# Optimization experiments

Hardware: AMD Instinct MI355X
Metric: run time of the kernel (lower is better)

## Reference

```python
import jax, jax.numpy as jnp
import numpy as np

B, S, H = 2, 2048, 1024
NH, HD = 16, 64  # num heads, head dim


def setup_inputs() -> dict:
    key = jax.random.key(0)
    ks = jax.random.split(key, 8)
    scale = 0.02
    return {
        "hidden_states": jax.random.normal(ks[0], (B, S, H), dtype=jnp.float32),
        "attention_mask": jnp.zeros((B, 1, 1, S), dtype=jnp.float32),
        "Wq": jax.random.normal(ks[1], (H, H), dtype=jnp.float32) * scale,
        "bq": jnp.zeros((H,), dtype=jnp.float32),
        "Wk": jax.random.normal(ks[2], (H, H), dtype=jnp.float32) * scale,
        "bk": jnp.zeros((H,), dtype=jnp.float32),
        "Wv": jax.random.normal(ks[3], (H, H), dtype=jnp.float32) * scale,
        "bv": jnp.zeros((H,), dtype=jnp.float32),
    }


def _split_heads(x):
    # [B,S,H] -> [B,NH,S,HD]
    b, s, _ = x.shape
    return x.reshape(b, s, NH, HD).transpose(0, 2, 1, 3)


def reference(hidden_states, attention_mask, Wq, bq, Wk, bk, Wv, bv):
    q = _split_heads(hidden_states @ Wq.T + bq)
    k = _split_heads(hidden_states @ Wk.T + bk)
    v = _split_heads(hidden_states @ Wv.T + bv)
    # scores: [B,NH,S,S]
    scores = jnp.einsum("bhqd,bhkd->bhqk", q, k) / jnp.sqrt(jnp.float32(HD))
    scores = scores + attention_mask
    att = jax.nn.softmax(scores, axis=-1)  # dropout is identity in eval
    ctx = jnp.einsum("bhqk,bhkd->bhqd", att, v)
    # [B,NH,S,HD] -> [B,S,H]
    return ctx.transpose(0, 2, 1, 3).reshape(hidden_states.shape[0], hidden_states.shape[1], NH * HD)
```

## Files before the change

kernel.cpp:

```cpp
#include <hip/hip_runtime.h>
#include <stdint.h>

#define BB 2
#define SS 2048
#define HH 1024
#define NH 16
#define HD 64

#define LOG2E 1.4426950408889634f
#define QSCALE (0.125f * LOG2E)

typedef short bfrag  __attribute__((ext_vector_type(8)));
typedef short bfrag4 __attribute__((ext_vector_type(4)));
typedef float f32x4  __attribute__((ext_vector_type(4)));

__device__ __forceinline__ short f2bf(float f) {
    union { float f; uint32_t u; } v; v.f = f;
    uint32_t r = (v.u + 0x7fffu + ((v.u >> 16) & 1u)) >> 16;
    return (short)r;
}

__device__ __forceinline__ uint32_t pack_bf16(float a, float b) {
#if __has_builtin(__builtin_amdgcn_cvt_pk_bf16_f32)
    auto t = __builtin_amdgcn_cvt_pk_bf16_f32(a, b);
    uint32_t u; __builtin_memcpy(&u, &t, 4);
    return u;
#else
    uint32_t ua = __float_as_uint(a) + 0x8000u;
    uint32_t ub = __float_as_uint(b) + 0x8000u;
    return __builtin_amdgcn_perm(ub, ua, 0x07060302u);
#endif
}

__global__ __launch_bounds__(256) void cvt_all(
    const float* __restrict__ X,  const float* __restrict__ Wq,
    const float* __restrict__ Wk, const float* __restrict__ Wv,
    const float* __restrict__ mask,
    short* __restrict__ Xb, short* __restrict__ Wcat,
    float* __restrict__ maskl)
{
    int i = blockIdx.x * 256 + threadIdx.x;
    if (i >= 1835008) {
        int off = i - 1835008;
        float4 f = ((const float4*)mask)[off];
        f.x *= LOG2E; f.y *= LOG2E; f.z *= LOG2E; f.w *= LOG2E;
        ((float4*)maskl)[off] = f;
        return;
    }
    const float* src; short* dst; int off;
    if (i < 1048576)      { src = X;  dst = Xb;                 off = i; }
    else if (i < 1310720) { src = Wq; dst = Wcat;               off = i - 1048576; }
    else if (i < 1572864) { src = Wk; dst = Wcat + 1048576;     off = i - 1310720; }
    else                  { src = Wv; dst = Wcat + 2097152;     off = i - 1572864; }
    float4 f = ((const float4*)src)[off];
    short4 s;
    s.x = f2bf(f.x); s.y = f2bf(f.y); s.z = f2bf(f.z); s.w = f2bf(f.w);
    ((short4*)dst)[off] = s;
}

__device__ __forceinline__ void gload_lds16(const void* g, void* lds) {
    __builtin_amdgcn_global_load_lds(
        (__attribute__((address_space(1))) void*)(uintptr_t)g,
        (__attribute__((address_space(3))) void*)(uintptr_t)lds,
        16, 0, 0);
}

__global__ __launch_bounds__(256, 3) void qkv_gemm(
    const short* __restrict__ X, const short* __restrict__ Wcat,
    const float* __restrict__ bq, const float* __restrict__ bk, const float* __restrict__ bv,
    short* __restrict__ Qo, short* __restrict__ Ko, short* __restrict__ Vo)
{
    __shared__ __align__(16) short smem[17408];

    const int tid  = threadIdx.x;
    const int wave = tid >> 6, lane = tid & 63;
    const int quad = lane >> 4, l15 = lane & 15;
    const int mTile = blockIdx.y * 128;
    const int nTile = blockIdx.x * 128;
    const int z = nTile >> 10;
    const int nLocT = nTile & 1023;
    const float* bias = (z == 0) ? bq : (z == 1) ? bk : bv;

    f32x4 acc[4][4];
#pragma unroll
    for (int i = 0; i < 4; ++i)
#pragma unroll
        for (int j = 0; j < 4; ++j) acc[i][j] = (f32x4)0.0f;

    const int srow  = lane >> 3;
    const int c_lin = lane & 7;
    const int mBase = (wave >> 1) * 64;
    const int nBase = (wave & 1) * 64;

    for (int k0 = 0; k0 < 1024; k0 += 64) {
        __syncthreads();
#pragma unroll
        for (int i = 0; i < 4; ++i) {
            int row = i * 32 + wave * 8 + srow;
            int cg  = c_lin ^ (row & 7);
            gload_lds16(X + (size_t)(mTile + row) * 1024 + k0 + cg * 8,
                        (char*)smem + i * 4096 + wave * 1024);
            gload_lds16(Wcat + (size_t)(nTile + row) * 1024 + k0 + cg * 8,
                        (char*)smem + 16384 + i * 4096 + wave * 1024);
        }
        __syncthreads();

#pragma unroll
        for (int kt = 0; kt < 2; ++kt) {
            bfrag af[4], bf[4];
#pragma unroll
            for (int t = 0; t < 4; ++t) {
                int arow = mBase + t * 16 + l15;
                int aslot = (kt * 4 + quad) ^ (arow & 7);
                af[t] = *(const bfrag*)((const char*)smem + arow * 128 + aslot * 16);
                int brow = nBase + t * 16 + l15;
                int bslot = (kt * 4 + quad) ^ (brow & 7);
                bf[t] = *(const bfrag*)((const char*)smem + 16384 + brow * 128 + bslot * 16);
            }
#pragma unroll
            for (int mt = 0; mt < 4; ++mt)
#pragma unroll
                for (int ct = 0; ct < 4; ++ct)
                    acc[mt][ct] = __builtin_amdgcn_mfma_f32_16x16x32_bf16(
                        af[mt], bf[ct], acc[mt][ct], 0, 0, 0);
        }
    }

    __syncthreads();
    const int b = mTile >> 11, sBase = mTile & 2047;

    if (z == 2) {
#pragma unroll
        for (int mt = 0; mt < 4; ++mt)
#pragma unroll
            for (int ct = 0; ct < 4; ++ct)
#pragma unroll
                for (int r = 0; r < 4; ++r) {
                    int nl = nBase + ct * 16 + l15;
                    int sl = mBase + mt * 16 + quad * 4 + r;
                    smem[nl * 136 + sl] = f2bf(acc[mt][ct][r] + bias[nLocT + nl]);
                }
        __syncthreads();
#pragma unroll
        for (int p = 0; p < 8; ++p) {
            int nl = p * 16 + (tid >> 4);
            int cg = tid & 15;
            int blk = cg >> 3;
            int c2  = cg & 7;
            int base = blk * 64 + (c2 >> 2) * 32 + (c2 & 3) * 4;
            int2 lo = *(const int2*)(smem + nl * 136 + base);
            int2 hi = *(const int2*)(smem + nl * 136 + base + 16);
            int4 v; v.x = lo.x; v.y = lo.y; v.z = hi.x; v.w = hi.y;
            int ng = nLocT + nl, hh = ng >> 6, d = ng & 63;
            *(int4*)(Vo + ((size_t)(b * 16 + hh) * 64 + d) * 2048 + sBase + cg * 8) = v;
        }
    } else {
        short* Out = (z == 0) ? Qo : Ko;
        float scale = (z == 0) ? QSCALE : 1.0f;
#pragma unroll
        for (int mt = 0; mt < 4; ++mt)
#pragma unroll
            for (int ct = 0; ct < 4; ++ct)
#pragma unroll
                for (int r = 0; r < 4; ++r) {
                    int ml = mBase + mt * 16 + quad * 4 + r;
                    int nl = nBase + ct * 16 + l15;
                    smem[ml * 136 + nl] = f2bf((acc[mt][ct][r] + bias[nLocT + nl]) * scale);
                }
        __syncthreads();
#pragma unroll
        for (int p = 0; p < 8; ++p) {
            int ml = p * 16 + (tid >> 4);
            int c  = tid & 15;
            bfrag v8 = *(const bfrag*)(smem + ml * 136 + c * 8);
            int s  = sBase + ml;
            int nl = nLocT + c * 8, hh = nl >> 6, d = nl & 63;
            *(bfrag*)(Out + (((size_t)(b * 16 + hh) << 11) + s) * 64 + d) = v8;
        }
    }
}

__global__ __launch_bounds__(256, 2) void attn_kernel(
    const short* __restrict__ Qb, const short* __restrict__ Kb, const short* __restrict__ Vb,
    const float* __restrict__ maskl, float* __restrict__ out)
{
    __shared__ __align__(16) char smem[32768];

    const int tid  = threadIdx.x;
    const int wave = tid >> 6, lane = tid & 63;
    const int quad = lane >> 4, l15 = lane & 15;

    const int id = blockIdx.x;
    const int slot = id >> 3;
    const int bh = ((id & 7) << 2) | (slot & 3);
    const int qt = slot >> 2;
    const int b  = bh >> 4, h = bh & 15;
    const int qBase = qt * 128 + wave * 32;

    int ksrc[2], vsrc[2];
#pragma unroll
    for (int i = 0; i < 2; ++i) {
        int ci = wave * 128 + i * 64 + lane;
        int r = ci >> 3, c = ci & 7;
        int cs = (c ^ (r & 7)) * 16;
        ksrc[i] = r * 128  + cs;
        vsrc[i] = r * 4096 + cs;
    }
    const char* kBase = (const char*)(Kb + (size_t)bh * SS * HD);
    const char* vBase = (const char*)(Vb + (size_t)bh * HD * SS);
    const char* mSrc  = (const char*)(maskl + b * SS) + quad * 16;

    const short* Qp = Qb + ((size_t)bh * SS + qBase) * HD;
    bfrag qf[2][2];
#pragma unroll
    for (int hf = 0; hf < 2; ++hf)
#pragma unroll
        for (int kt = 0; kt < 2; ++kt)
            qf[hf][kt] = *(const bfrag*)(Qp + (size_t)(hf * 16 + l15) * HD + kt * 32 + quad * 8);

    int kAddr[2];
#pragma unroll
    for (int kt = 0; kt < 2; ++kt)
        kAddr[kt] = l15 * 128 + (((kt * 4 + quad) ^ (l15 & 7)) * 16);
    int vAddr[2];
#pragma unroll
    for (int g = 0; g < 2; ++g)
        vAddr[g] = 8192 + l15 * 128 + (((g * 4 + quad) ^ (l15 & 7)) * 16);

    const f32x4 z4 = (f32x4)0.0f;
    const bfrag ones8 = {0x3F80, 0x3F80, 0x3F80, 0x3F80,
                         0x3F80, 0x3F80, 0x3F80, 0x3F80};

    f32x4 oacc[2][4], ol[2];
#pragma unroll
    for (int hf = 0; hf < 2; ++hf) {
        ol[hf] = z4;
#pragma unroll
        for (int dt = 0; dt < 4; ++dt) oacc[hf][dt] = z4;
    }

#pragma unroll
    for (int i = 0; i < 2; ++i) {
        gload_lds16(kBase + ksrc[i], smem + wave * 2048 + i * 1024);
        gload_lds16(vBase + vsrc[i], smem + 8192 + wave * 2048 + i * 1024);
    }

    auto astep = [&](int CUR, int NXT, int jn, int pref) {
        __syncthreads();
        if (pref) {
#pragma unroll
            for (int i = 0; i < 2; ++i) {
                gload_lds16(kBase + jn * 8192 + ksrc[i], smem + NXT + wave * 2048 + i * 1024);
                gload_lds16(vBase + jn * 128  + vsrc[i], smem + NXT + 8192 + wave * 2048 + i * 1024);
            }
        }

        f32x4 mvl[4];
#pragma unroll
        for (int ct = 0; ct < 4; ++ct)
            mvl[ct] = *(const f32x4*)(mSrc + ct * 64);
        mSrc += 256;

        f32x4 s0[4], s1[4];
#pragma unroll
        for (int ct = 0; ct < 4; ++ct) {
            bfrag kf0 = *(const bfrag*)(smem + CUR + kAddr[0] + ct * 2048);
            bfrag kf1 = *(const bfrag*)(smem + CUR + kAddr[1] + ct * 2048);
            s0[ct] = __builtin_amdgcn_mfma_f32_16x16x32_bf16(kf0, qf[0][0], mvl[ct], 0, 0, 0);
            s0[ct] = __builtin_amdgcn_mfma_f32_16x16x32_bf16(kf1, qf[0][1], s0[ct],  0, 0, 0);
            s1[ct] = __builtin_amdgcn_mfma_f32_16x16x32_bf16(kf0, qf[1][0], mvl[ct], 0, 0, 0);
            s1[ct] = __builtin_amdgcn_mfma_f32_16x16x32_bf16(kf1, qf[1][1], s1[ct],  0, 0, 0);
        }

        bfrag p0[2], p1[2];
#pragma unroll
        for (int g = 0; g < 2; ++g) {
            union { uint32_t u[4]; bfrag v; } cvt;
            cvt.u[0] = pack_bf16(__builtin_amdgcn_exp2f(s0[2*g][0]),   __builtin_amdgcn_exp2f(s0[2*g][1]));
            cvt.u[1] = pack_bf16(__builtin_amdgcn_exp2f(s0[2*g][2]),   __builtin_amdgcn_exp2f(s0[2*g][3]));
            cvt.u[2] = pack_bf16(__builtin_amdgcn_exp2f(s0[2*g+1][0]), __builtin_amdgcn_exp2f(s0[2*g+1][1]));
            cvt.u[3] = pack_bf16(__builtin_amdgcn_exp2f(s0[2*g+1][2]), __builtin_amdgcn_exp2f(s0[2*g+1][3]));
            p0[g] = cvt.v;
            cvt.u[0] = pack_bf16(__builtin_amdgcn_exp2f(s1[2*g][0]),   __builtin_amdgcn_exp2f(s1[2*g][1]));
            cvt.u[1] = pack_bf16(__builtin_amdgcn_exp2f(s1[2*g][2]),   __builtin_amdgcn_exp2f(s1[2*g][3]));
            cvt.u[2] = pack_bf16(__builtin_amdgcn_exp2f(s1[2*g+1][0]), __builtin_amdgcn_exp2f(s1[2*g+1][1]));
            cvt.u[3] = pack_bf16(__builtin_amdgcn_exp2f(s1[2*g+1][2]), __builtin_amdgcn_exp2f(s1[2*g+1][3]));
            p1[g] = cvt.v;
        }

#pragma unroll
        for (int dt = 0; dt < 4; ++dt) {
#pragma unroll
            for (int g = 0; g < 2; ++g) {
                bfrag v = *(const bfrag*)(smem + CUR + vAddr[g] + dt * 2048);
                oacc[0][dt] = __builtin_amdgcn_mfma_f32_16x16x32_bf16(p0[g], v, oacc[0][dt], 0, 0, 0);
                oacc[1][dt] = __builtin_amdgcn_mfma_f32_16x16x32_bf16(p1[g], v, oacc[1][dt], 0, 0, 0);
            }
        }
#pragma unroll
        for (int g = 0; g < 2; ++g) {
            ol[0] = __builtin_amdgcn_mfma_f32_16x16x32_bf16(p0[g], ones8, ol[0], 0, 0, 0);
            ol[1] = __builtin_amdgcn_mfma_f32_16x16x32_bf16(p1[g], ones8, ol[1], 0, 0, 0);
        }
    };

    for (int jj = 0; jj < 16; ++jj) {
        astep(0,     16384, 2 * jj + 1, 1);
        astep(16384, 0,     2 * jj + 2, jj < 15);
    }

#pragma unroll
    for (int hf = 0; hf < 2; ++hf) {
#pragma unroll
        for (int r = 0; r < 4; ++r) {
            float linv = 1.0f / ol[hf][r];
            int qrow = qBase + hf * 16 + quad * 4 + r;
#pragma unroll
            for (int dt = 0; dt < 4; ++dt)
                out[((size_t)(b * SS + qrow)) * HH + h * 64 + dt * 16 + l15] =
                    oacc[hf][dt][r] * linv;
        }
    }
}

extern "C" void kernel_launch(void* const* d_in, const int* in_sizes, int n_in,
                              void* d_out, int out_size, void* d_ws, size_t ws_size,
                              hipStream_t stream) {
    const float* hs   = (const float*)d_in[0];
    const float* mask = (const float*)d_in[1];
    const float* Wq   = (const float*)d_in[2];
    const float* bq   = (const float*)d_in[3];
    const float* Wk   = (const float*)d_in[4];
    const float* bk   = (const float*)d_in[5];
    const float* Wv   = (const float*)d_in[6];
    const float* bv   = (const float*)d_in[7];
    float* out = (float*)d_out;

    char* ws = (char*)d_ws;
    short* Xb    = (short*)(ws);
    short* Wcat  = (short*)(ws + (8ull  << 20));
    short* Qb    = (short*)(ws + (14ull << 20));
    short* Kb    = (short*)(ws + (22ull << 20));
    short* Vb    = (short*)(ws + (30ull << 20));
    float* maskl = (float*)(ws + (38ull << 20));

    cvt_all<<<7172, 256, 0, stream>>>(hs, Wq, Wk, Wv, mask, Xb, Wcat, maskl);

    qkv_gemm<<<dim3(24, 32), 256, 0, stream>>>(Xb, Wcat, bq, bk, bv, Qb, Kb, Vb);

    attn_kernel<<<512, 256, 0, stream>>>(Qb, Kb, Vb, maskl, out);
}
```

Before: 157.9 us.

## Double KV tile to 128 keys per step and add MFMA priority hints

The attention kernel now processes 128 keys per pipeline step instead of 64. K/V shared tiles double to 64KB of LDS with a 16-way XOR swizzle for V, so half as many barriers and async prefetches are issued. It also wraps the MFMA phases in s_setprio to favour matrix issue, and batches V fragment loads ahead of their MFMAs. The larger LDS footprint (64KB per block) may limit the two-blocks-per-CU occupancy, and the extra live score registers raise register pressure.

```diff
diff --git a/kernel.cpp b/kernel.cpp
--- a/kernel.cpp
+++ b/kernel.cpp
@@ -184,7 +184,7 @@
     const short* __restrict__ Qb, const short* __restrict__ Kb, const short* __restrict__ Vb,
     const float* __restrict__ maskl, float* __restrict__ out)
 {
-    __shared__ __align__(16) char smem[32768];
+    __shared__ __align__(16) char smem[65536];
 
     const int tid  = threadIdx.x;
     const int wave = tid >> 6, lane = tid & 63;
@@ -197,14 +197,14 @@
     const int b  = bh >> 4, h = bh & 15;
     const int qBase = qt * 128 + wave * 32;
 
-    int ksrc[2], vsrc[2];
-#pragma unroll
-    for (int i = 0; i < 2; ++i) {
-        int ci = wave * 128 + i * 64 + lane;
-        int r = ci >> 3, c = ci & 7;
-        int cs = (c ^ (r & 7)) * 16;
-        ksrc[i] = r * 128  + cs;
-        vsrc[i] = r * 4096 + cs;
+    int ksrc[4], vsrc[4];
+#pragma unroll
+    for (int i = 0; i < 4; ++i) {
+        int ci = wave * 256 + i * 64 + lane;
+        int kr = ci >> 3, kc = ci & 7;
+        ksrc[i] = kr * 128 + ((kc ^ (kr & 7)) * 16);
+        int vr = ci >> 4, vc = ci & 15;
+        vsrc[i] = vr * 4096 + ((vc ^ (vr & 15)) * 16);
     }
     const char* kBase = (const char*)(Kb + (size_t)bh * SS * HD);
     const char* vBase = (const char*)(Vb + (size_t)bh * HD * SS);
@@ -222,10 +222,12 @@
 #pragma unroll
     for (int kt = 0; kt < 2; ++kt)
         kAddr[kt] = l15 * 128 + (((kt * 4 + quad) ^ (l15 & 7)) * 16);
-    int vAddr[2];
-#pragma unroll
-    for (int g = 0; g < 2; ++g)
-        vAddr[g] = 8192 + l15 * 128 + (((g * 4 + quad) ^ (l15 & 7)) * 16);
+    int vAddr[2][2];
+#pragma unroll
+    for (int a = 0; a < 2; ++a)
+#pragma unroll
+        for (int g = 0; g < 2; ++g)
+            vAddr[a][g] = 16384 + l15 * 256 + (((a * 8 + g * 4 + quad) ^ l15) * 16);
 
     const f32x4 z4 = (f32x4)0.0f;
     const bfrag ones8 = {0x3F80, 0x3F80, 0x3F80, 0x3F80,
@@ -240,73 +242,85 @@
     }
 
 #pragma unroll
-    for (int i = 0; i < 2; ++i) {
-        gload_lds16(kBase + ksrc[i], smem + wave * 2048 + i * 1024);
-        gload_lds16(vBase + vsrc[i], smem + 8192 + wave * 2048 + i * 1024);
+    for (int i = 0; i < 4; ++i) {
+        gload_lds16(kBase + ksrc[i], smem + wave * 4096 + i * 1024);
+        gload_lds16(vBase + vsrc[i], smem + 16384 + wave * 4096 + i * 1024);
     }
 
     auto astep = [&](int CUR, int NXT, int jn, int pref) {
         __syncthreads();
         if (pref) {
 #pragma unroll
-            for (int i = 0; i < 2; ++i) {
-                gload_lds16(kBase + jn * 8192 + ksrc[i], smem + NXT + wave * 2048 + i * 1024);
-                gload_lds16(vBase + jn * 128  + vsrc[i], smem + NXT + 8192 + wave * 2048 + i * 1024);
-            }
-        }
-
-        f32x4 mvl[4];
-#pragma unroll
-        for (int ct = 0; ct < 4; ++ct)
-            mvl[ct] = *(const f32x4*)(mSrc + ct * 64);
-        mSrc += 256;
-
-        f32x4 s0[4], s1[4];
-#pragma unroll
-        for (int ct = 0; ct < 4; ++ct) {
-            bfrag kf0 = *(const bfrag*)(smem + CUR + kAddr[0] + ct * 2048);
-            bfrag kf1 = *(const bfrag*)(smem + CUR + kAddr[1] + ct * 2048);
-            s0[ct] = __builtin_amdgcn_mfma_f32_16x16x32_bf16(kf0, qf[0][0], mvl[ct], 0, 0, 0);
-            s0[ct] = __builtin_amdgcn_mfma_f32_16x16x32_bf16(kf1, qf[0][1], s0[ct],  0, 0, 0);
-            s1[ct] = __builtin_amdgcn_mfma_f32_16x16x32_bf16(kf0, qf[1][0], mvl[ct], 0, 0, 0);
-            s1[ct] = __builtin_amdgcn_mfma_f32_16x16x32_bf16(kf1, qf[1][1], s1[ct],  0, 0, 0);
-        }
-
-        bfrag p0[2], p1[2];
-#pragma unroll
-        for (int g = 0; g < 2; ++g) {
-            union { uint32_t u[4]; bfrag v; } cvt;
-            cvt.u[0] = pack_bf16(__builtin_amdgcn_exp2f(s0[2*g][0]),   __builtin_amdgcn_exp2f(s0[2*g][1]));
-            cvt.u[1] = pack_bf16(__builtin_amdgcn_exp2f(s0[2*g][2]),   __builtin_amdgcn_exp2f(s0[2*g][3]));
-            cvt.u[2] = pack_bf16(__builtin_amdgcn_exp2f(s0[2*g+1][0]), __builtin_amdgcn_exp2f(s0[2*g+1][1]));
-            cvt.u[3] = pack_bf16(__builtin_amdgcn_exp2f(s0[2*g+1][2]), __builtin_amdgcn_exp2f(s0[2*g+1][3]));
-            p0[g] = cvt.v;
-            cvt.u[0] = pack_bf16(__builtin_amdgcn_exp2f(s1[2*g][0]),   __builtin_amdgcn_exp2f(s1[2*g][1]));
-            cvt.u[1] = pack_bf16(__builtin_amdgcn_exp2f(s1[2*g][2]),   __builtin_amdgcn_exp2f(s1[2*g][3]));
-            cvt.u[2] = pack_bf16(__builtin_amdgcn_exp2f(s1[2*g+1][0]), __builtin_amdgcn_exp2f(s1[2*g+1][1]));
-            cvt.u[3] = pack_bf16(__builtin_amdgcn_exp2f(s1[2*g+1][2]), __builtin_amdgcn_exp2f(s1[2*g+1][3]));
-            p1[g] = cvt.v;
-        }
-
-#pragma unroll
-        for (int dt = 0; dt < 4; ++dt) {
+            for (int i = 0; i < 4; ++i) {
+                gload_lds16(kBase + (size_t)jn * 16384 + ksrc[i],
+                            smem + NXT + wave * 4096 + i * 1024);
+                gload_lds16(vBase + (size_t)jn * 256 + vsrc[i],
+                            smem + NXT + 16384 + wave * 4096 + i * 1024);
+            }
+        }
+
+        f32x4 s0[2][4], s1[2][4];
+        __builtin_amdgcn_s_setprio(1);
+#pragma unroll
+        for (int a = 0; a < 2; ++a) {
+            f32x4 mvl[4];
+#pragma unroll
+            for (int ct = 0; ct < 4; ++ct)
+                mvl[ct] = *(const f32x4*)(mSrc + a * 256 + ct * 64);
+#pragma unroll
+            for (int ct = 0; ct < 4; ++ct) {
+                bfrag kf0 = *(const bfrag*)(smem + CUR + a * 8192 + kAddr[0] + ct * 2048);
+                bfrag kf1 = *(const bfrag*)(smem + CUR + a * 8192 + kAddr[1] + ct * 2048);
+                s0[a][ct] = __builtin_amdgcn_mfma_f32_16x16x32_bf16(kf0, qf[0][0], mvl[ct], 0, 0, 0);
+                s0[a][ct] = __builtin_amdgcn_mfma_f32_16x16x32_bf16(kf1, qf[0][1], s0[a][ct], 0, 0, 0);
+                s1[a][ct] = __builtin_amdgcn_mfma_f32_16x16x32_bf16(kf0, qf[1][0], mvl[ct], 0, 0, 0);
+                s1[a][ct] = __builtin_amdgcn_mfma_f32_16x16x32_bf16(kf1, qf[1][1], s1[a][ct], 0, 0, 0);
+            }
+        }
+        __builtin_amdgcn_s_setprio(0);
+        mSrc += 512;
+
+        bfrag p0[2][2], p1[2][2];
+#pragma unroll
+        for (int a = 0; a < 2; ++a)
 #pragma unroll
             for (int g = 0; g < 2; ++g) {
-                bfrag v = *(const bfrag*)(smem + CUR + vAddr[g] + dt * 2048);
-                oacc[0][dt] = __builtin_amdgcn_mfma_f32_16x16x32_bf16(p0[g], v, oacc[0][dt], 0, 0, 0);
-                oacc[1][dt] = __builtin_amdgcn_mfma_f32_16x16x32_bf16(p1[g], v, oacc[1][dt], 0, 0, 0);
-            }
-        }
-#pragma unroll
-        for (int g = 0; g < 2; ++g) {
-            ol[0] = __builtin_amdgcn_mfma_f32_16x16x32_bf16(p0[g], ones8, ol[0], 0, 0, 0);
-            ol[1] = __builtin_amdgcn_mfma_f32_16x16x32_bf16(p1[g], ones8, ol[1], 0, 0, 0);
-        }
+                union { uint32_t u[4]; bfrag v; } cvt;
+                cvt.u[0] = pack_bf16(__builtin_amdgcn_exp2f(s0[a][2*g][0]),   __builtin_amdgcn_exp2f(s0[a][2*g][1]));
+                cvt.u[1] = pack_bf16(__builtin_amdgcn_exp2f(s0[a][2*g][2]),   __builtin_amdgcn_exp2f(s0[a][2*g][3]));
+                cvt.u[2] = pack_bf16(__builtin_amdgcn_exp2f(s0[a][2*g+1][0]), __builtin_amdgcn_exp2f(s0[a][2*g+1][1]));
+                cvt.u[3] = pack_bf16(__builtin_amdgcn_exp2f(s0[a][2*g+1][2]), __builtin_amdgcn_exp2f(s0[a][2*g+1][3]));
+                p0[a][g] = cvt.v;
+                cvt.u[0] = pack_bf16(__builtin_amdgcn_exp2f(s1[a][2*g][0]),   __builtin_amdgcn_exp2f(s1[a][2*g][1]));
+                cvt.u[1] = pack_bf16(__builtin_amdgcn_exp2f(s1[a][2*g][2]),   __builtin_amdgcn_exp2f(s1[a][2*g][3]));
+                cvt.u[2] = pack_bf16(__builtin_amdgcn_exp2f(s1[a][2*g+1][0]), __builtin_amdgcn_exp2f(s1[a][2*g+1][1]));
+                cvt.u[3] = pack_bf16(__builtin_amdgcn_exp2f(s1[a][2*g+1][2]), __builtin_amdgcn_exp2f(s1[a][2*g+1][3]));
+                p1[a][g] = cvt.v;
+            }
+
+        __builtin_amdgcn_s_setprio(1);
+#pragma unroll
+        for (int a = 0; a < 2; ++a)
+#pragma unroll
+            for (int g = 0; g < 2; ++g) {
+                bfrag vv[4];
+#pragma unroll
+                for (int dt = 0; dt < 4; ++dt)
+                    vv[dt] = *(const bfrag*)(smem + CUR + vAddr[a][g] + dt * 4096);
+#pragma unroll
+                for (int dt = 0; dt < 4; ++dt) {
+                    oacc[0][dt] = __builtin_amdgcn_mfma_f32_16x16x32_bf16(p0[a][g], vv[dt], oacc[0][dt], 0, 0, 0);
+                    oacc[1][dt] = __builtin_amdgcn_mfma_f32_16x16x32_bf16(p1[a][g], vv[dt], oacc[1][dt], 0, 0, 0);
+                }
+                ol[0] = __builtin_amdgcn_mfma_f32_16x16x32_bf16(p0[a][g], ones8, ol[0], 0, 0, 0);
+                ol[1] = __builtin_amdgcn_mfma_f32_16x16x32_bf16(p1[a][g], ones8, ol[1], 0, 0, 0);
+            }
+        __builtin_amdgcn_s_setprio(0);
     };
 
-    for (int jj = 0; jj < 16; ++jj) {
-        astep(0,     16384, 2 * jj + 1, 1);
-        astep(16384, 0,     2 * jj + 2, jj < 15);
+    for (int jj = 0; jj < 8; ++jj) {
+        astep(0,     32768, 2 * jj + 1, 1);
+        astep(32768, 0,     2 * jj + 2, jj < 7);
     }
 
 #pragma unroll
```

Result: no change. 156.0 us (-1.2%).

## Halve attention query tile, double grid, stage mask in LDS, add setprio

Applied to the files above, without the earlier changes.

The attention kernel now handles 64 query rows per block (16 per wave) instead of 128, so the grid doubles to 1024 blocks and launch bounds allow 4 blocks per CU. The aim is more resident waves per CU to hide latency, and fewer registers per wave. The mask row is copied once into an extra 8 KB of LDS instead of being read from global memory every step. s_setprio is raised around the MFMA sections to favour matrix issue. In exchange, each K/V tile loaded into LDS serves half as many query rows, which doubles K/V global and LDS traffic per unit of work.

```diff
diff --git a/kernel.cpp b/kernel.cpp
--- a/kernel.cpp
+++ b/kernel.cpp
@@ -180,11 +180,11 @@
     }
 }
 
-__global__ __launch_bounds__(256, 2) void attn_kernel(
+__global__ __launch_bounds__(256, 4) void attn_kernel(
     const short* __restrict__ Qb, const short* __restrict__ Kb, const short* __restrict__ Vb,
     const float* __restrict__ maskl, float* __restrict__ out)
 {
-    __shared__ __align__(16) char smem[32768];
+    __shared__ __align__(16) char smem[40960];
 
     const int tid  = threadIdx.x;
     const int wave = tid >> 6, lane = tid & 63;
@@ -195,7 +195,7 @@
     const int bh = ((id & 7) << 2) | (slot & 3);
     const int qt = slot >> 2;
     const int b  = bh >> 4, h = bh & 15;
-    const int qBase = qt * 128 + wave * 32;
+    const int qBase = qt * 64 + wave * 16;
 
     int ksrc[2], vsrc[2];
 #pragma unroll
@@ -208,15 +208,12 @@
     }
     const char* kBase = (const char*)(Kb + (size_t)bh * SS * HD);
     const char* vBase = (const char*)(Vb + (size_t)bh * HD * SS);
-    const char* mSrc  = (const char*)(maskl + b * SS) + quad * 16;
 
     const short* Qp = Qb + ((size_t)bh * SS + qBase) * HD;
-    bfrag qf[2][2];
-#pragma unroll
-    for (int hf = 0; hf < 2; ++hf)
-#pragma unroll
-        for (int kt = 0; kt < 2; ++kt)
-            qf[hf][kt] = *(const bfrag*)(Qp + (size_t)(hf * 16 + l15) * HD + kt * 32 + quad * 8);
+    bfrag qf[2];
+#pragma unroll
+    for (int kt = 0; kt < 2; ++kt)
+        qf[kt] = *(const bfrag*)(Qp + (size_t)l15 * HD + kt * 32 + quad * 8);
 
     int kAddr[2];
 #pragma unroll
@@ -231,77 +228,77 @@
     const bfrag ones8 = {0x3F80, 0x3F80, 0x3F80, 0x3F80,
                          0x3F80, 0x3F80, 0x3F80, 0x3F80};
 
-    f32x4 oacc[2][4], ol[2];
-#pragma unroll
-    for (int hf = 0; hf < 2; ++hf) {
-        ol[hf] = z4;
-#pragma unroll
-        for (int dt = 0; dt < 4; ++dt) oacc[hf][dt] = z4;
-    }
+    f32x4 oacc[4], ol = z4;
+#pragma unroll
+    for (int dt = 0; dt < 4; ++dt) oacc[dt] = z4;
 
 #pragma unroll
     for (int i = 0; i < 2; ++i) {
         gload_lds16(kBase + ksrc[i], smem + wave * 2048 + i * 1024);
         gload_lds16(vBase + vsrc[i], smem + 8192 + wave * 2048 + i * 1024);
     }
+#pragma unroll
+    for (int i = 0; i < 2; ++i) {
+        int ci = wave * 128 + i * 64 + lane;
+        gload_lds16((const char*)(maskl + b * SS) + ci * 16,
+                    smem + 32768 + wave * 2048 + i * 1024);
+    }
+
+    int mOff = 32768 + quad * 16;
 
     auto astep = [&](int CUR, int NXT, int jn, int pref) {
         __syncthreads();
         if (pref) {
 #pragma unroll
             for (int i = 0; i < 2; ++i) {
-                gload_lds16(kBase + jn * 8192 + ksrc[i], smem + NXT + wave * 2048 + i * 1024);
-                gload_lds16(vBase + jn * 128  + vsrc[i], smem + NXT + 8192 + wave * 2048 + i * 1024);
+                gload_lds16(kBase + (size_t)jn * 8192 + ksrc[i],
+                            smem + NXT + wave * 2048 + i * 1024);
+                gload_lds16(vBase + (size_t)jn * 128 + vsrc[i],
+                            smem + NXT + 8192 + wave * 2048 + i * 1024);
             }
         }
 
         f32x4 mvl[4];
 #pragma unroll
         for (int ct = 0; ct < 4; ++ct)
-            mvl[ct] = *(const f32x4*)(mSrc + ct * 64);
-        mSrc += 256;
-
-        f32x4 s0[4], s1[4];
+            mvl[ct] = *(const f32x4*)(smem + mOff + ct * 64);
+        mOff += 256;
+
+        f32x4 s[4];
+        __builtin_amdgcn_s_setprio(1);
 #pragma unroll
         for (int ct = 0; ct < 4; ++ct) {
             bfrag kf0 = *(const bfrag*)(smem + CUR + kAddr[0] + ct * 2048);
             bfrag kf1 = *(const bfrag*)(smem + CUR + kAddr[1] + ct * 2048);
-            s0[ct] = __builtin_amdgcn_mfma_f32_16x16x32_bf16(kf0, qf[0][0], mvl[ct], 0, 0, 0);
-            s0[ct] = __builtin_amdgcn_mfma_f32_16x16x32_bf16(kf1, qf[0][1], s0[ct],  0, 0, 0);
-            s1[ct] = __builtin_amdgcn_mfma_f32_16x16x32_bf16(kf0, qf[1][0], mvl[ct], 0, 0, 0);
-            s1[ct] = __builtin_amdgcn_mfma_f32_16x16x32_bf16(kf1, qf[1][1], s1[ct],  0, 0, 0);
-        }
-
-        bfrag p0[2], p1[2];
+            s[ct] = __builtin_amdgcn_mfma_f32_16x16x32_bf16(kf0, qf[0], mvl[ct], 0, 0, 0);
+            s[ct] = __builtin_amdgcn_mfma_f32_16x16x32_bf16(kf1, qf[1], s[ct],  0, 0, 0);
+        }
+        __builtin_amdgcn_s_setprio(0);
+
+        bfrag p[2];
 #pragma unroll
         for (int g = 0; g < 2; ++g) {
             union { uint32_t u[4]; bfrag v; } cvt;
-            cvt.u[0] = pack_bf16(__builtin_amdgcn_exp2f(s0[2*g][0]),   __builtin_amdgcn_exp2f(s0[2*g][1]));
-            cvt.u[1] = pack_bf16(__builtin_amdgcn_exp2f(s0[2*g][2]),   __builtin_amdgcn_exp2f(s0[2*g][3]));
-            cvt.u[2] = pack_bf16(__builtin_amdgcn_exp2f(s0[2*g+1][0]), __builtin_amdgcn_exp2f(s0[2*g+1][1]));
-            cvt.u[3] = pack_bf16(__builtin_amdgcn_exp2f(s0[2*g+1][2]), __builtin_amdgcn_exp2f(s0[2*g+1][3]));
-            p0[g] = cvt.v;
-            cvt.u[0] = pack_bf16(__builtin_amdgcn_exp2f(s1[2*g][0]),   __builtin_amdgcn_exp2f(s1[2*g][1]));
-            cvt.u[1] = pack_bf16(__builtin_amdgcn_exp2f(s1[2*g][2]),   __builtin_amdgcn_exp2f(s1[2*g][3]));
-            cvt.u[2] = pack_bf16(__builtin_amdgcn_exp2f(s1[2*g+1][0]), __builtin_amdgcn_exp2f(s1[2*g+1][1]));
-            cvt.u[3] = pack_bf16(__builtin_amdgcn_exp2f(s1[2*g+1][2]), __builtin_amdgcn_exp2f(s1[2*g+1][3]));
-            p1[g] = cvt.v;
-        }
-
-#pragma unroll
-        for (int dt = 0; dt < 4; ++dt) {
-#pragma unroll
-            for (int g = 0; g < 2; ++g) {
-                bfrag v = *(const bfrag*)(smem + CUR + vAddr[g] + dt * 2048);
-                oacc[0][dt] = __builtin_amdgcn_mfma_f32_16x16x32_bf16(p0[g], v, oacc[0][dt], 0, 0, 0);
-                oacc[1][dt] = __builtin_amdgcn_mfma_f32_16x16x32_bf16(p1[g], v, oacc[1][dt], 0, 0, 0);
-            }
-        }
+            cvt.u[0] = pack_bf16(__builtin_amdgcn_exp2f(s[2*g][0]),   __builtin_amdgcn_exp2f(s[2*g][1]));
+            cvt.u[1] = pack_bf16(__builtin_amdgcn_exp2f(s[2*g][2]),   __builtin_amdgcn_exp2f(s[2*g][3]));
+            cvt.u[2] = pack_bf16(__builtin_amdgcn_exp2f(s[2*g+1][0]), __builtin_amdgcn_exp2f(s[2*g+1][1]));
+            cvt.u[3] = pack_bf16(__builtin_amdgcn_exp2f(s[2*g+1][2]), __builtin_amdgcn_exp2f(s[2*g+1][3]));
+            p[g] = cvt.v;
+        }
+
+        __builtin_amdgcn_s_setprio(1);
 #pragma unroll
         for (int g = 0; g < 2; ++g) {
-            ol[0] = __builtin_amdgcn_mfma_f32_16x16x32_bf16(p0[g], ones8, ol[0], 0, 0, 0);
-            ol[1] = __builtin_amdgcn_mfma_f32_16x16x32_bf16(p1[g], ones8, ol[1], 0, 0, 0);
-        }
+            bfrag vv[4];
+#pragma unroll
+            for (int dt = 0; dt < 4; ++dt)
+                vv[dt] = *(const bfrag*)(smem + CUR + vAddr[g] + dt * 2048);
+#pragma unroll
+            for (int dt = 0; dt < 4; ++dt)
+                oacc[dt] = __builtin_amdgcn_mfma_f32_16x16x32_bf16(p[g], vv[dt], oacc[dt], 0, 0, 0);
+            ol = __builtin_amdgcn_mfma_f32_16x16x32_bf16(p[g], ones8, ol, 0, 0, 0);
+        }
+        __builtin_amdgcn_s_setprio(0);
     };
 
     for (int jj = 0; jj < 16; ++jj) {
@@ -310,16 +307,13 @@
     }
 
 #pragma unroll
-    for (int hf = 0; hf < 2; ++hf) {
-#pragma unroll
-        for (int r = 0; r < 4; ++r) {
-            float linv = 1.0f / ol[hf][r];
-            int qrow = qBase + hf * 16 + quad * 4 + r;
-#pragma unroll
-            for (int dt = 0; dt < 4; ++dt)
-                out[((size_t)(b * SS + qrow)) * HH + h * 64 + dt * 16 + l15] =
-                    oacc[hf][dt][r] * linv;
-        }
+    for (int r = 0; r < 4; ++r) {
+        float linv = 1.0f / ol[r];
+        int qrow = qBase + quad * 4 + r;
+#pragma unroll
+        for (int dt = 0; dt < 4; ++dt)
+            out[((size_t)(b * SS + qrow)) * HH + h * 64 + dt * 16 + l15] =
+                oacc[dt][r] * linv;
     }
 }
 
@@ -348,5 +342,5 @@
 
     qkv_gemm<<<dim3(24, 32), 256, 0, stream>>>(Xb, Wcat, bq, bk, bv, Qb, Kb, Vb);
 
-    attn_kernel<<<512, 256, 0, stream>>>(Qb, Kb, Vb, maskl, out);
-}
+    attn_kernel<<<1024, 256, 0, stream>>>(Qb, Kb, Vb, maskl, out);
+}
```

Result: slower. 162.7 us (+3.1%).

## Split attention KV range across two wave groups per block with LDS reduction

Applied to the files above, without the earlier changes.

Doubles the attention block to 512 threads. The two 4-wave groups each process half of the key/value sequence for the same 128 query rows, using separate LDS double buffers, and their partial outputs and row sums are combined through LDS at the end. This doubles the number of waves available to hide latency without raising the grid size. It also raises wave priority around the MFMA sections. The cost is 64KB of LDS per block, an extra reduction pass, and possibly lower block occupancy per CU.

```diff
diff --git a/kernel.cpp b/kernel.cpp
--- a/kernel.cpp
+++ b/kernel.cpp
@@ -180,27 +180,32 @@
     }
 }
 
-__global__ __launch_bounds__(256, 2) void attn_kernel(
+__global__ __launch_bounds__(512, 4) void attn_kernel(
     const short* __restrict__ Qb, const short* __restrict__ Kb, const short* __restrict__ Vb,
     const float* __restrict__ maskl, float* __restrict__ out)
 {
-    __shared__ __align__(16) char smem[32768];
+    __shared__ __align__(16) char smem[65536];
 
     const int tid  = threadIdx.x;
     const int wave = tid >> 6, lane = tid & 63;
     const int quad = lane >> 4, l15 = lane & 15;
+    const int grp  = wave >> 2;
+    const int gw   = wave & 3;
 
     const int id = blockIdx.x;
     const int slot = id >> 3;
     const int bh = ((id & 7) << 2) | (slot & 3);
     const int qt = slot >> 2;
     const int b  = bh >> 4, h = bh & 15;
-    const int qBase = qt * 128 + wave * 32;
+    const int qBase = qt * 128 + gw * 32;
+
+    const int gBase = grp * 32768;
+    const int t0 = grp * 16;
 
     int ksrc[2], vsrc[2];
 #pragma unroll
     for (int i = 0; i < 2; ++i) {
-        int ci = wave * 128 + i * 64 + lane;
+        int ci = gw * 128 + i * 64 + lane;
         int r = ci >> 3, c = ci & 7;
         int cs = (c ^ (r & 7)) * 16;
         ksrc[i] = r * 128  + cs;
@@ -208,7 +213,7 @@
     }
     const char* kBase = (const char*)(Kb + (size_t)bh * SS * HD);
     const char* vBase = (const char*)(Vb + (size_t)bh * HD * SS);
-    const char* mSrc  = (const char*)(maskl + b * SS) + quad * 16;
+    const char* mSrc  = (const char*)(maskl + b * SS + grp * 1024) + quad * 16;
 
     const short* Qp = Qb + ((size_t)bh * SS + qBase) * HD;
     bfrag qf[2][2];
@@ -221,11 +226,11 @@
     int kAddr[2];
 #pragma unroll
     for (int kt = 0; kt < 2; ++kt)
-        kAddr[kt] = l15 * 128 + (((kt * 4 + quad) ^ (l15 & 7)) * 16);
+        kAddr[kt] = gBase + l15 * 128 + (((kt * 4 + quad) ^ (l15 & 7)) * 16);
     int vAddr[2];
 #pragma unroll
     for (int g = 0; g < 2; ++g)
-        vAddr[g] = 8192 + l15 * 128 + (((g * 4 + quad) ^ (l15 & 7)) * 16);
+        vAddr[g] = gBase + 8192 + l15 * 128 + (((g * 4 + quad) ^ (l15 & 7)) * 16);
 
     const f32x4 z4 = (f32x4)0.0f;
     const bfrag ones8 = {0x3F80, 0x3F80, 0x3F80, 0x3F80,
@@ -241,8 +246,8 @@
 
 #pragma unroll
     for (int i = 0; i < 2; ++i) {
-        gload_lds16(kBase + ksrc[i], smem + wave * 2048 + i * 1024);
-        gload_lds16(vBase + vsrc[i], smem + 8192 + wave * 2048 + i * 1024);
+        gload_lds16(kBase + (size_t)t0 * 8192 + ksrc[i], smem + gBase + gw * 2048 + i * 1024);
+        gload_lds16(vBase + (size_t)t0 * 128  + vsrc[i], smem + gBase + 8192 + gw * 2048 + i * 1024);
     }
 
     auto astep = [&](int CUR, int NXT, int jn, int pref) {
@@ -250,8 +255,10 @@
         if (pref) {
 #pragma unroll
             for (int i = 0; i < 2; ++i) {
-                gload_lds16(kBase + jn * 8192 + ksrc[i], smem + NXT + wave * 2048 + i * 1024);
-                gload_lds16(vBase + jn * 128  + vsrc[i], smem + NXT + 8192 + wave * 2048 + i * 1024);
+                gload_lds16(kBase + (size_t)jn * 8192 + ksrc[i],
+                            smem + gBase + NXT + gw * 2048 + i * 1024);
+                gload_lds16(vBase + (size_t)jn * 128  + vsrc[i],
+                            smem + gBase + NXT + 8192 + gw * 2048 + i * 1024);
             }
         }
 
@@ -262,6 +269,7 @@
         mSrc += 256;
 
         f32x4 s0[4], s1[4];
+        __builtin_amdgcn_s_setprio(1);
 #pragma unroll
         for (int ct = 0; ct < 4; ++ct) {
             bfrag kf0 = *(const bfrag*)(smem + CUR + kAddr[0] + ct * 2048);
@@ -271,6 +279,7 @@
             s1[ct] = __builtin_amdgcn_mfma_f32_16x16x32_bf16(kf0, qf[1][0], mvl[ct], 0, 0, 0);
             s1[ct] = __builtin_amdgcn_mfma_f32_16x16x32_bf16(kf1, qf[1][1], s1[ct],  0, 0, 0);
         }
+        __builtin_amdgcn_s_setprio(0);
 
         bfrag p0[2], p1[2];
 #pragma unroll
@@ -288,6 +297,7 @@
             p1[g] = cvt.v;
         }
 
+        __builtin_amdgcn_s_setprio(1);
 #pragma unroll
         for (int dt = 0; dt < 4; ++dt) {
 #pragma unroll
@@ -302,24 +312,44 @@
             ol[0] = __builtin_amdgcn_mfma_f32_16x16x32_bf16(p0[g], ones8, ol[0], 0, 0, 0);
             ol[1] = __builtin_amdgcn_mfma_f32_16x16x32_bf16(p1[g], ones8, ol[1], 0, 0, 0);
         }
+        __builtin_amdgcn_s_setprio(0);
     };
 
-    for (int jj = 0; jj < 16; ++jj) {
-        astep(0,     16384, 2 * jj + 1, 1);
-        astep(16384, 0,     2 * jj + 2, jj < 15);
-    }
-
-#pragma unroll
-    for (int hf = 0; hf < 2; ++hf) {
-#pragma unroll
-        for (int r = 0; r < 4; ++r) {
-            float linv = 1.0f / ol[hf][r];
-            int qrow = qBase + hf * 16 + quad * 4 + r;
-#pragma unroll
-            for (int dt = 0; dt < 4; ++dt)
-                out[((size_t)(b * SS + qrow)) * HH + h * 64 + dt * 16 + l15] =
-                    oacc[hf][dt][r] * linv;
-        }
+    for (int jj = 0; jj < 8; ++jj) {
+        astep(0,     16384, t0 + 2 * jj + 1, 1);
+        astep(16384, 0,     t0 + 2 * jj + 2, jj < 7);
+    }
+
+    __syncthreads();
+    float* Op = (float*)smem;
+    float* lp = (float*)(smem + 34816);
+
+    if (grp == 1) {
+#pragma unroll
+        for (int hf = 0; hf < 2; ++hf)
+#pragma unroll
+            for (int r = 0; r < 4; ++r) {
+                int row = gw * 32 + hf * 16 + quad * 4 + r;
+                lp[row] = ol[hf][r];
+#pragma unroll
+                for (int dt = 0; dt < 4; ++dt)
+                    Op[row * 68 + dt * 16 + l15] = oacc[hf][dt][r];
+            }
+    }
+    __syncthreads();
+    if (grp == 0) {
+#pragma unroll
+        for (int hf = 0; hf < 2; ++hf)
+#pragma unroll
+            for (int r = 0; r < 4; ++r) {
+                int row = gw * 32 + hf * 16 + quad * 4 + r;
+                float linv = 1.0f / (ol[hf][r] + lp[row]);
+                int qrow = qBase + hf * 16 + quad * 4 + r;
+#pragma unroll
+                for (int dt = 0; dt < 4; ++dt)
+                    out[((size_t)(b * SS + qrow)) * HH + h * 64 + dt * 16 + l15] =
+                        (oacc[hf][dt][r] + Op[row * 68 + dt * 16 + l15]) * linv;
+            }
     }
 }
 
@@ -348,5 +378,5 @@
 
     qkv_gemm<<<dim3(24, 32), 256, 0, stream>>>(Xb, Wcat, bq, bk, bv, Qb, Kb, Vb);
 
-    attn_kernel<<<512, 256, 0, stream>>>(Qb, Kb, Vb, maskl, out);
-}
+    attn_kernel<<<512, 512, 0, stream>>>(Qb, Kb, Vb, maskl, out);
+}
```

After: 169.7 us. 1.08x slower.
